# Performance work log

Measured on AMD Instinct MI355X. Metric: run time of the kernel, lower is better.

Reference implementation:

```python
import jax, jax.numpy as jnp
import numpy as np

B, L, E, H, D, DFF = 2, 2048, 1024, 16, 64, 4096
SCALE = D ** 0.5


def rmsnorm(x):
    # NOTE: original uses mean(x*x)**0.5 with no eps and no learned scale
    rms = jnp.sqrt(jnp.mean(x * x, axis=-1, keepdims=True))
    return x / rms


def alibi_matrix():
    i = jnp.arange(L)
    dists = -jnp.abs(i[None, :] - i[:, None]).astype(jnp.float32)  # [L, L]
    slopes = 2.0 ** (-jnp.linspace(1.0, 8.0, H))                   # [H]
    alibi = slopes[:, None, None] * dists                          # [H, L, L]
    causal = jnp.tril(jnp.ones((L, L), dtype=bool))
    return jnp.where(causal[None], alibi, -jnp.inf)[None]          # [1, H, L, L]


def setup_inputs() -> dict:
    key = jax.random.key(0)
    ks = jax.random.split(key, 16)
    s = 0.02
    return {
        "X": jax.random.normal(ks[0], (B, L, E), jnp.float32),
        "encoder_out": jax.random.normal(ks[1], (B, L, E), jnp.float32),
        # self-attention params
        "Wqkv": jax.random.normal(ks[2], (E, 3 * H * D), jnp.float32) * s,
        "bqkv": jnp.zeros((3 * H * D,), jnp.float32),
        "Wo_sa": jax.random.normal(ks[3], (H * D, E), jnp.float32) * s,
        "bo_sa": jnp.zeros((E,), jnp.float32),
        # cross-attention params (computed by torch module but its forward returns X, so unused)
        "Wq": jax.random.normal(ks[4], (E, H * D), jnp.float32) * s,
        "bq": jnp.zeros((H * D,), jnp.float32),
        "Wkv": jax.random.normal(ks[5], (E, 2 * H * D), jnp.float32) * s,
        "bkv": jnp.zeros((2 * H * D,), jnp.float32),
        "Wo_ca": jax.random.normal(ks[6], (H * D, E), jnp.float32) * s,
        "bo_ca": jnp.zeros((E,), jnp.float32),
        # GLU FFN params (bias=False)
        "Ww": jax.random.normal(ks[7], (E, DFF), jnp.float32) * s,
        "Wv": jax.random.normal(ks[8], (E, DFF), jnp.float32) * s,
        "Wout": jax.random.normal(ks[9], (DFF, E), jnp.float32) * s,
    }


def reference(X, encoder_out, Wqkv, bqkv, Wo_sa, bo_sa, Wq, bq, Wkv, bkv,
              Wo_ca, bo_ca, Ww, Wv, Wout):
    alibi = alibi_matrix()

    # ---- self-attention (pre-norm + residual) ----
    h = rmsnorm(X)
    qkv = (h @ Wqkv + bqkv).reshape(B, L, H, 3, D)
    Q, K, V = qkv[..., 0, :], qkv[..., 1, :], qkv[..., 2, :]      # [B, L, H, D]
    scores = jnp.einsum('blhd,bmhd->bhlm', Q, K) / SCALE + alibi  # [B, H, L, L]
    attn = jax.nn.softmax(scores, axis=-1)
    ctx = jnp.einsum('bhlm,bmhd->blhd', attn, V).reshape(B, L, H * D)
    X = X + ctx @ Wo_sa + bo_sa

    # ---- cross-attention stage ----
    # Faithful to source: CrossAttention.forward returns its input X (the
    # normalized tensor) rather than the attention output, so this block is
    # X + rmsnorm(X). Cross-attn params never affect the output.
    X = X + rmsnorm(X)

    # ---- GLU FFN (pre-norm + residual), exact (erf) GELU as in torch F.gelu ----
    h = rmsnorm(X)
    ff = jax.nn.gelu(h @ Ww, approximate=False) * (h @ Wv)
    X = X + ff @ Wout
    return X
```

## Files before the change

kernel.cpp:

```cpp
#include <hip/hip_runtime.h>

#define B_SZ 2
#define L_SEQ 2048
#define E_DIM 1024
#define NH 16
#define DH 64
#define DFF_DIM 4096
#define ROWS (B_SZ * L_SEQ)
#define NCID 80

typedef __attribute__((ext_vector_type(8))) short short8;
typedef __attribute__((ext_vector_type(4))) float f32x4;

__device__ __forceinline__ short f2bf(float f) {
  unsigned u = __builtin_bit_cast(unsigned, f);
  u = (u + 0x7FFFu + ((u >> 16) & 1u)) >> 16;
  return (short)u;
}
__device__ __forceinline__ float bf2f(short s) {
  unsigned u = ((unsigned)(unsigned short)s) << 16;
  return __builtin_bit_cast(float, u);
}

__device__ __forceinline__ float fast_gelu(float x) {
  float ax = fabsf(x) * 0.70710678118654752f;
  float t = __builtin_amdgcn_rcpf(__builtin_fmaf(0.3275911f, ax, 1.0f));
  float p = t * __builtin_fmaf(
                    t,
                    __builtin_fmaf(
                        t,
                        __builtin_fmaf(t,
                                       __builtin_fmaf(t, 1.061405429f,
                                                      -1.453152027f),
                                       1.421413741f),
                        -0.284496736f),
                    0.254829592f);
  float erf = 1.0f - p * __expf(-ax * ax);
  erf = copysignf(erf, x);
  return 0.5f * x * (1.0f + erf);
}

__device__ __forceinline__ void async_copy16(const void* g, void* l) {
  __builtin_amdgcn_global_load_lds(
      (const __attribute__((address_space(1))) void*)g,
      (__attribute__((address_space(3))) void*)l, 16, 0, 0);
}

__device__ __forceinline__ float block_sum256(float v) {
  __shared__ float sbuf[4];
#pragma unroll
  for (int off = 32; off > 0; off >>= 1) v += __shfl_xor(v, off, 64);
  int lane = threadIdx.x & 63, w = threadIdx.x >> 6;
  if (lane == 0) sbuf[w] = v;
  __syncthreads();
  return sbuf[0] + sbuf[1] + sbuf[2] + sbuf[3];
}

__global__ __launch_bounds__(256) void prep_all(
    const float* __restrict__ Wqkv, const float* __restrict__ Wo,
    const float* __restrict__ Ww, const float* __restrict__ Wv,
    const float* __restrict__ Wout, const float* __restrict__ X,
    short* __restrict__ Bqkv3, short* __restrict__ WoT,
    short* __restrict__ Bcat, short* __restrict__ WoutT,
    short* __restrict__ H) {
  __shared__ float tile[32][33];
  int b = blockIdx.x;
  if (b < 16384) {
    const float* W;
    short* Wt;
    int K, N, mode, bx, by;
    if (b < 3072) {
      W = Wqkv; Wt = Bqkv3; K = 1024; N = 3072; mode = 1;
      bx = b % 96; by = b / 96;
    } else if (b < 4096) {
      int c = b - 3072;
      W = Wo; Wt = WoT; K = 1024; N = 1024; mode = 1;
      bx = c & 31; by = c >> 5;
    } else if (b < 8192) {
      int c = b - 4096;
      W = Ww; Wt = Bcat; K = 1024; N = 4096; mode = 2;
      bx = c & 127; by = c >> 7;
    } else if (b < 12288) {
      int c = b - 8192;
      W = Wv; Wt = Bcat; K = 1024; N = 4096; mode = 3;
      bx = c & 127; by = c >> 7;
    } else {
      int c = b - 12288;
      W = Wout; Wt = WoutT; K = 4096; N = 1024; mode = 1;
      bx = c & 31; by = c >> 5;
    }
    int n0 = bx * 32, k0 = by * 32;
    int tx = threadIdx.x & 31, ty = threadIdx.x >> 5;
#pragma unroll
    for (int i = 0; i < 4; i++)
      tile[ty + 8 * i][tx] = W[(size_t)(k0 + ty + 8 * i) * N + n0 + tx];
    __syncthreads();
#pragma unroll
    for (int i = 0; i < 4; i++) {
      int n = n0 + ty + 8 * i;
      int orow = (mode == 1)
                     ? n
                     : ((n >> 5) * 64 + (n & 31) + (mode == 3 ? 32 : 0));
      Wt[(size_t)orow * K + k0 + tx] = f2bf(tile[tx][ty + 8 * i]);
    }
  } else {
    size_t row = b - 16384;
    float4 v = ((const float4*)(X + row * E_DIM))[threadIdx.x];
    float ss = v.x * v.x + v.y * v.y + v.z * v.z + v.w * v.w;
    ss = block_sum256(ss);
    float inv = rsqrtf(ss * (1.0f / E_DIM));
    short* h = H + row * E_DIM + (size_t)threadIdx.x * 4;
    h[0] = f2bf(v.x * inv);
    h[1] = f2bf(v.y * inv);
    h[2] = f2bf(v.z * inv);
    h[3] = f2bf(v.w * inv);
  }
}

__global__ __launch_bounds__(256) void resid_rms_fused(
    const float* __restrict__ X, const float* __restrict__ P0,
    const float* __restrict__ P1, const float* __restrict__ bias,
    float* __restrict__ Xout, short* __restrict__ H) {
  size_t row = blockIdx.x;
  int t = threadIdx.x;
  float4 v = ((const float4*)(X + row * E_DIM))[t];
  float4 a = ((const float4*)(P0 + row * E_DIM))[t];
  float4 b = ((const float4*)(P1 + row * E_DIM))[t];
  float4 c = ((const float4*)bias)[t];
  v.x += a.x + b.x + c.x;
  v.y += a.y + b.y + c.y;
  v.z += a.z + b.z + c.z;
  v.w += a.w + b.w + c.w;
  float ss = v.x * v.x + v.y * v.y + v.z * v.z + v.w * v.w;
  ss = block_sum256(ss);
  float inv = rsqrtf(ss * (1.0f / E_DIM));
  float4 o;
  o.x = v.x * (1.0f + inv);
  o.y = v.y * (1.0f + inv);
  o.z = v.z * (1.0f + inv);
  o.w = v.w * (1.0f + inv);
  ((float4*)(Xout + row * E_DIM))[t] = o;
  short* h = H + row * E_DIM + (size_t)t * 4;
  h[0] = f2bf(v.x * inv);
  h[1] = f2bf(v.y * inv);
  h[2] = f2bf(v.z * inv);
  h[3] = f2bf(v.w * inv);
}

__global__ __launch_bounds__(256) void add2_k(const float* __restrict__ P0,
                                              const float* __restrict__ P1,
                                              float* __restrict__ out) {
  size_t i = (size_t)blockIdx.x * 256 + threadIdx.x;
  float4 v = ((const float4*)out)[i];
  float4 a = ((const float4*)P0)[i];
  float4 b = ((const float4*)P1)[i];
  v.x += a.x + b.x;
  v.y += a.y + b.y;
  v.z += a.z + b.z;
  v.w += a.w + b.w;
  ((float4*)out)[i] = v;
}

__global__ __launch_bounds__(256, 2) void gemm_bt(
    const short* __restrict__ A, const short* __restrict__ Bt,
    const float* __restrict__ bias, void* __restrict__ out,
    void* __restrict__ out2, void* __restrict__ out3, int M, int N, int K,
    int epi, int ksplit) {
  __shared__ short smem[128 * 32 * 4];
  short* As0 = smem;
  short* Bs0 = smem + 4096;
  short* As1 = smem + 8192;
  short* Bs1 = smem + 12288;
  int t = threadIdx.x;
  int lane = t & 63;
  int quad = lane >> 4, l16 = lane & 15;
  int wave = t >> 6;
  int wr = wave >> 1, wc = wave & 1;
  int m0 = blockIdx.y * 128, n0 = blockIdx.x * 128;
  int klen = K / ksplit;
  int kstart = blockIdx.z * klen;

  f32x4 acc[4][4];
#pragma unroll
  for (int i = 0; i < 4; i++)
#pragma unroll
    for (int j = 0; j < 4; j++) acc[i][j] = (f32x4){0.f, 0.f, 0.f, 0.f};

  for (int k0 = kstart; k0 < kstart + klen; k0 += 64) {
    __syncthreads();
#pragma unroll
    for (int p = 0; p < 2; p++) {
      int s = p * 256 + t;
      int mm = s >> 2, kk = (s & 3) * 8;
      const short* ag = A + (size_t)(m0 + mm) * K + k0 + kk;
      const short* bg = Bt + (size_t)(n0 + mm) * K + k0 + kk;
      async_copy16(ag, As0 + (size_t)s * 8);
      async_copy16(bg, Bs0 + (size_t)s * 8);
      async_copy16(ag + 32, As1 + (size_t)s * 8);
      async_copy16(bg + 32, Bs1 + (size_t)s * 8);
    }
    __syncthreads();
#pragma unroll
    for (int half = 0; half < 2; half++) {
      const short* As = half ? As1 : As0;
      const short* Bs = half ? Bs1 : Bs0;
      short8 af[4], bfv[4];
#pragma unroll
      for (int i = 0; i < 4; i++) {
        af[i] = *(const short8*)&As[(wr * 64 + i * 16 + l16) * 32 + quad * 8];
        bfv[i] = *(const short8*)&Bs[(wc * 64 + i * 16 + l16) * 32 + quad * 8];
      }
#pragma unroll
      for (int mi = 0; mi < 4; mi++)
#pragma unroll
        for (int ni = 0; ni < 4; ni++)
          acc[mi][ni] = __builtin_amdgcn_mfma_f32_16x16x32_bf16(
              af[mi], bfv[ni], acc[mi][ni], 0, 0, 0);
    }
  }

  if (epi == 5) {
    short* FF = (short*)out;
    int ffbase = blockIdx.x * 64 + wc * 32;
#pragma unroll
    for (int mi = 0; mi < 4; mi++)
#pragma unroll
      for (int ni = 0; ni < 2; ni++)
#pragma unroll
        for (int r = 0; r < 4; r++) {
          int rowl = wr * 64 + mi * 16 + quad * 4 + r;
          float g = fast_gelu(acc[mi][ni][r]);
          FF[(size_t)(m0 + rowl) * DFF_DIM + ffbase + ni * 16 + l16] =
              f2bf(g * acc[mi][ni + 2][r]);
        }
    return;
  }

#pragma unroll
  for (int mi = 0; mi < 4; mi++) {
#pragma unroll
    for (int ni = 0; ni < 4; ni++) {
      int col = n0 + wc * 64 + ni * 16 + l16;
#pragma unroll
      for (int r = 0; r < 4; r++) {
        int row = m0 + wr * 64 + mi * 16 + quad * 4 + r;
        float v = acc[mi][ni][r];
        if (epi == 4) {
          float* po = (float*)out + (size_t)blockIdx.z * ((size_t)M * N);
          po[(size_t)row * N + col] = v;
        } else {
          v += bias[col];
          int h = col / 192;
          int rem = col - h * 192;
          int ty = rem >> 6, d = rem & 63;
          short* dst = (ty == 0) ? (short*)out
                                 : ((ty == 1) ? (short*)out2 : (short*)out3);
          int bb = row >> 11, l = row & 2047;
          dst[((size_t)(bb * NH + h) * L_SEQ + l) * DH + d] = f2bf(v);
        }
      }
    }
  }
}

__global__ __launch_bounds__(256) void v_transp(const short* __restrict__ Vh,
                                                short* __restrict__ VTh) {
  int lt = blockIdx.x, bh = blockIdx.y;
  __shared__ short vtile[64 * 72];
  int t = threadIdx.x;
  int r = t >> 3, c = (t & 7) * 8;
  const short* src = Vh + ((size_t)bh * L_SEQ + lt * 64) * DH;
#pragma unroll
  for (int p = 0; p < 2; p++) {
    int row = r + p * 32;
    short8 vv = *(const short8*)(src + (size_t)row * DH + c);
    *(short8*)&vtile[row * 72 + c] = vv;
  }
  __syncthreads();
#pragma unroll
  for (int p = 0; p < 2; p++) {
    int d = r + p * 32;
    short8 o;
#pragma unroll
    for (int u = 0; u < 8; u++) o[u] = vtile[(c + u) * 72 + d];
    *(short8*)(VTh + ((size_t)bh * DH + d) * L_SEQ + lt * 64 + c) = o;
  }
}

__global__ __launch_bounds__(256) void attn_k(const short* __restrict__ Qh,
                                              const short* __restrict__ Kh,
                                              const short* __restrict__ VTh,
                                              float* __restrict__ OP,
                                              float* __restrict__ RS) {
  int cid = blockIdx.x;
  int bh = blockIdx.y;
  int b = bh >> 4, h = bh & 15;
  int qt, ch;
  if (cid < 8) {
    qt = cid; ch = 0;
  } else if (cid < 24) {
    qt = 8 + ((cid - 8) >> 1); ch = (cid - 8) & 1;
  } else if (cid < 48) {
    qt = 16 + (cid - 24) / 3; ch = (cid - 24) % 3;
  } else {
    qt = 24 + ((cid - 48) >> 2); ch = (cid - 48) & 3;
  }
  int t0 = ch * 8;
  int tend = min(t0 + 8, qt + 1);

  int t = threadIdx.x;
  int wave = t >> 6, lane = t & 63;
  int quad = lane >> 4, l16 = lane & 15;

  __shared__ short kt[64 * 72];
  __shared__ short vt[64 * 72];
  __shared__ short pb[4 * 16 * 70];

  const float slope = exp2f(-(1.0f + (7.0f / 15.0f) * (float)h));
  int iw = qt * 64 + wave * 16;

  short8 qf[2];
  {
    const short* qp = Qh + ((size_t)bh * L_SEQ + iw + l16) * DH + quad * 8;
    qf[0] = *(const short8*)(qp);
    qf[1] = *(const short8*)(qp + 32);
  }

  f32x4 o[4];
#pragma unroll
  for (int i = 0; i < 4; i++) o[i] = (f32x4){0.f, 0.f, 0.f, 0.f};
  float rs[4] = {0.f, 0.f, 0.f, 0.f};
  float crow[4];
  int irow[4];
#pragma unroll
  for (int r = 0; r < 4; r++) {
    irow[r] = iw + quad * 4 + r;
    crow[r] = -slope * (float)irow[r] - 8.0f;
  }

  int sr = t >> 3, sc = (t & 7) * 8;
  const short* kg = Kh + (size_t)bh * L_SEQ * DH;
  const short* vg = VTh + (size_t)bh * DH * L_SEQ;
  short8 kreg[2], vreg[2];
  auto loadKV = [&](int j0) {
    kreg[0] = *(const short8*)(kg + (size_t)(j0 + sr) * DH + sc);
    kreg[1] = *(const short8*)(kg + (size_t)(j0 + sr + 32) * DH + sc);
    vreg[0] = *(const short8*)(vg + (size_t)sr * L_SEQ + j0 + sc);
    vreg[1] = *(const short8*)(vg + (size_t)(sr + 32) * L_SEQ + j0 + sc);
  };
  loadKV(t0 * 64);

  short* pw = &pb[wave * 16 * 70];
  for (int tix = t0; tix < tend; ++tix) {
    int j0 = tix * 64;
    __syncthreads();
    *(short8*)&kt[sr * 72 + sc] = kreg[0];
    *(short8*)&kt[(sr + 32) * 72 + sc] = kreg[1];
    *(short8*)&vt[sr * 72 + sc] = vreg[0];
    *(short8*)&vt[(sr + 32) * 72 + sc] = vreg[1];
    __syncthreads();
    if (tix + 1 < tend) loadKV(j0 + 64);

    f32x4 s[4];
#pragma unroll
    for (int nt = 0; nt < 4; nt++) {
      f32x4 a = (f32x4){0.f, 0.f, 0.f, 0.f};
#pragma unroll
      for (int ks = 0; ks < 2; ks++) {
        short8 bf =
            *(const short8*)&kt[(nt * 16 + l16) * 72 + ks * 32 + quad * 8];
        a = __builtin_amdgcn_mfma_f32_16x16x32_bf16(qf[ks], bf, a, 0, 0, 0);
      }
      s[nt] = a;
    }
    bool diag = (tix == qt);
#pragma unroll
    for (int nt = 0; nt < 4; nt++) {
      int j = j0 + nt * 16 + l16;
      float jb = slope * (float)j;
#pragma unroll
      for (int r = 0; r < 4; r++) {
        float v = __builtin_fmaf(s[nt][r], 0.125f, jb + crow[r]);
        if (diag && j > irow[r]) v = -1e30f;
        float p = __expf(v);
        rs[r] += p;
        pw[(quad * 4 + r) * 70 + nt * 16 + l16] = f2bf(p);
      }
    }
    short8 pf[2];
    pf[0] = *(const short8*)&pw[l16 * 70 + quad * 8];
    pf[1] = *(const short8*)&pw[l16 * 70 + 32 + quad * 8];
#pragma unroll
    for (int nt = 0; nt < 4; nt++) {
#pragma unroll
      for (int ks = 0; ks < 2; ks++) {
        short8 bv =
            *(const short8*)&vt[(nt * 16 + l16) * 72 + ks * 32 + quad * 8];
        o[nt] = __builtin_amdgcn_mfma_f32_16x16x32_bf16(pf[ks], bv, o[nt], 0,
                                                        0, 0);
      }
    }
  }
  float* op = OP + ((size_t)bh * NCID + cid) * 64 * 64;
  float* rsp = RS + ((size_t)bh * NCID + cid) * 64;
#pragma unroll
  for (int r = 0; r < 4; r++) {
#pragma unroll
    for (int off = 1; off < 16; off <<= 1) rs[r] += __shfl_xor(rs[r], off, 64);
    int rowl = wave * 16 + quad * 4 + r;
#pragma unroll
    for (int nt = 0; nt < 4; nt++) op[rowl * 64 + nt * 16 + l16] = o[nt][r];
    if (l16 == 0) rsp[rowl] = rs[r];
  }
}

__global__ __launch_bounds__(256) void attn_merge(const float* __restrict__ OP,
                                                  const float* __restrict__ RS,
                                                  short* __restrict__ ctx) {
  int row = blockIdx.x;
  int b = row >> 11, i = row & 2047;
  int qt = i >> 6, rowin = i & 63;
  int base, nch;
  if (qt < 8) {
    base = qt; nch = 1;
  } else if (qt < 16) {
    base = 8 + 2 * (qt - 8); nch = 2;
  } else if (qt < 24) {
    base = 24 + 3 * (qt - 16); nch = 3;
  } else {
    base = 48 + 4 * (qt - 24); nch = 4;
  }
  int t = threadIdx.x;
  int col = t * 4;
  int h = col >> 6;
  int bh = b * NH + h;
  float4 o = {0.f, 0.f, 0.f, 0.f};
  float l = 0.f;
  for (int s = 0; s < nch; s++) {
    size_t cb = ((size_t)bh * NCID + base + s) * 64 + rowin;
    float4 v = *(const float4*)&OP[cb * 64 + (col & 63)];
    o.x += v.x;
    o.y += v.y;
    o.z += v.z;
    o.w += v.w;
    l += RS[cb];
  }
  float inv = 1.0f / l;
  short* dst = ctx + (size_t)row * (NH * DH) + col;
  dst[0] = f2bf(o.x * inv);
  dst[1] = f2bf(o.y * inv);
  dst[2] = f2bf(o.z * inv);
  dst[3] = f2bf(o.w * inv);
}

extern "C" void kernel_launch(void* const* d_in, const int* in_sizes, int n_in,
                              void* d_out, int out_size, void* d_ws,
                              size_t ws_size, hipStream_t stream) {
  const float* X = (const float*)d_in[0];
  const float* Wqkv = (const float*)d_in[2];
  const float* bqkv = (const float*)d_in[3];
  const float* Wo_sa = (const float*)d_in[4];
  const float* bo_sa = (const float*)d_in[5];
  const float* Ww = (const float*)d_in[12];
  const float* Wv = (const float*)d_in[13];
  const float* Wout = (const float*)d_in[14];

  char* ws = (char*)d_ws;
  auto take = [&](size_t bytes) {
    char* p = ws;
    ws += (bytes + 255) & ~(size_t)255;
    return p;
  };
  short* Bqkv3 = (short*)take((size_t)3072 * 1024 * 2);
  short* WoT = (short*)take((size_t)E_DIM * E_DIM * 2);
  short* Bcat = (short*)take((size_t)2 * DFF_DIM * E_DIM * 2);
  short* WoutT = (short*)take((size_t)E_DIM * DFF_DIM * 2);
  short* Hbuf = (short*)take((size_t)ROWS * E_DIM * 2);
  short* Qh = (short*)take((size_t)ROWS * NH * DH * 2);
  short* Kh = (short*)take((size_t)ROWS * NH * DH * 2);
  short* Vh = (short*)take((size_t)ROWS * NH * DH * 2);
  short* VTh = (short*)take((size_t)ROWS * NH * DH * 2);
  short* CTX = (short*)take((size_t)ROWS * NH * DH * 2);
  char* big = take((size_t)48 * 1024 * 1024);
  float* OP = (float*)big;
  float* RS = OP + (size_t)B_SZ * NH * NCID * 64 * 64;
  float* Pwo = (float*)(big + (size_t)16 * 1024 * 1024);
  short* FF = (short*)Pwo;
  float* Pwout = (float*)Qh;
  (void)ws_size;
  (void)in_sizes;
  (void)n_in;
  (void)out_size;

  dim3 blk(256);
  prep_all<<<16384 + ROWS, blk, 0, stream>>>(Wqkv, Wo_sa, Ww, Wv, Wout, X,
                                             Bqkv3, WoT, Bcat, WoutT, Hbuf);
  gemm_bt<<<dim3(3072 / 128, ROWS / 128), blk, 0, stream>>>(
      Hbuf, Bqkv3, bqkv, Qh, Kh, Vh, ROWS, 3072, 1024, 6, 1);
  v_transp<<<dim3(L_SEQ / 64, B_SZ * NH), blk, 0, stream>>>(Vh, VTh);
  attn_k<<<dim3(NCID, B_SZ * NH), blk, 0, stream>>>(Qh, Kh, VTh, OP, RS);
  attn_merge<<<ROWS, blk, 0, stream>>>(OP, RS, CTX);
  gemm_bt<<<dim3(1024 / 128, ROWS / 128, 2), blk, 0, stream>>>(
      CTX, WoT, nullptr, Pwo, nullptr, nullptr, ROWS, 1024, 1024, 4, 2);
  resid_rms_fused<<<ROWS, blk, 0, stream>>>(
      X, Pwo, Pwo + (size_t)ROWS * E_DIM, bo_sa, (float*)d_out, Hbuf);
  gemm_bt<<<dim3(2 * DFF_DIM / 128, ROWS / 128), blk, 0, stream>>>(
      Hbuf, Bcat, nullptr, FF, nullptr, nullptr, ROWS, 2 * DFF_DIM, 1024, 5,
      1);
  gemm_bt<<<dim3(1024 / 128, ROWS / 128, 2), blk, 0, stream>>>(
      FF, WoutT, nullptr, Pwout, nullptr, nullptr, ROWS, 1024, 4096, 4, 2);
  add2_k<<<ROWS * E_DIM / (256 * 4), blk, 0, stream>>>(
      Pwout, Pwout + (size_t)ROWS * E_DIM, (float*)d_out);
}
```

Before: 421.6 us.

## Add 256x256-tile pipelined MFMA GEMM for QKV and GLU up-projections

Introduces a new 512-thread GEMM kernel with 256x256 output tiles and 128-deep K steps. It uses swizzled LDS staging with async global-to-LDS copies, an 8-phase software pipeline interleaving loads with bf16 MFMAs, and s_setprio around the compute. It replaces the 128-tile gemm_bt for the QKV projection (head-split bias epilogue) and the fused GELU-gated FFN up-projection, to raise arithmetic intensity per byte of LDS and global traffic. The kernel uses 128KB of LDS, so one block fits per CU. The QKV launch also gets fewer blocks than there are CUs, which risks lower occupancy and poor load balance.

```diff
diff --git a/kernel.cpp b/kernel.cpp
--- a/kernel.cpp
+++ b/kernel.cpp
@@ -263,6 +263,163 @@
   }
 }
 
+__global__ __launch_bounds__(512, 2) void gemm256(
+    const short* __restrict__ A, const short* __restrict__ Bt,
+    const float* __restrict__ bias, void* __restrict__ out,
+    void* __restrict__ out2, void* __restrict__ out3, int M, int N, int K,
+    int epi) {
+  __shared__ __align__(16) short smem[65536];
+  (void)M;
+  (void)N;
+  int t = threadIdx.x;
+  int lane = t & 63;
+  int quad = lane >> 4, l16 = lane & 15;
+  int wave = t >> 6;
+  int wr = wave >> 2;
+  int wc = wave & 3;
+  int m0 = blockIdx.y * 256, n0 = blockIdx.x * 256;
+
+  int row0 = t >> 3;
+  int sl = (t & 7) ^ (row0 & 7);
+  int goff = row0 * K + sl * 8;
+  int ldw = t * 16;
+  char* smc = (char*)smem;
+  auto stageHT = [&](const short* gsrc, int ldsbase) {
+    async_copy16(gsrc + goff, smc + ldsbase + ldw);
+    async_copy16(gsrc + goff + (K << 6), smc + ldsbase + 8192 + ldw);
+  };
+
+  int swz = (l16 & 7) << 4;
+  int colp0 = (quad * 16) ^ swz;
+  int colp1 = (64 + quad * 16) ^ swz;
+  const char* aB = smc + wr * 16384 + l16 * 128;
+  const char* bB = smc + 32768 + (wc >> 1) * 16384 + (wc & 1) * 8192 +
+                   l16 * 128;
+
+  f32x4 acc[8][4];
+#pragma unroll
+  for (int i = 0; i < 8; i++)
+#pragma unroll
+    for (int j = 0; j < 4; j++) acc[i][j] = (f32x4){0.f, 0.f, 0.f, 0.f};
+  short8 areg[4][2], breg[4][2];
+
+  const short* Am0 = A + (size_t)m0 * K;
+  const short* Am1 = A + (size_t)(m0 + 128) * K;
+  const short* Bn0 = Bt + (size_t)n0 * K;
+  const short* Bn1 = Bt + (size_t)(n0 + 128) * K;
+
+  stageHT(Am0, 0);
+  stageHT(Am1, 16384);
+  stageHT(Bn0, 32768);
+  stageHT(Bn1, 49152);
+  stageHT(Bn0 + 64, 98304);
+  stageHT(Bn1 + 64, 114688);
+  asm volatile("s_waitcnt vmcnt(4)" ::: "memory");
+  __builtin_amdgcn_s_barrier();
+
+  int NJ = K >> 7;
+  for (int j = 0; j < NJ; ++j) {
+    int kb = j << 7;
+    bool lastI = (j == NJ - 1);
+#pragma unroll
+    for (int ph = 0; ph < 8; ++ph) {
+      const int sub = ph & 3;
+      const int mq = sub >> 1;
+      const int nq = sub & 1;
+      const int dOff = (ph >> 2) ? 65536 : 0;
+      if (sub == 0 || sub == 2) {
+#pragma unroll
+        for (int im = 0; im < 4; ++im) {
+          areg[im][0] =
+              *(const short8*)(aB + dOff + (mq * 4 + im) * 2048 + colp0);
+          areg[im][1] =
+              *(const short8*)(aB + dOff + (mq * 4 + im) * 2048 + colp1);
+        }
+      }
+      if (sub <= 1) {
+#pragma unroll
+        for (int in = 0; in < 2; ++in) {
+          breg[nq * 2 + in][0] =
+              *(const short8*)(bB + dOff + (nq * 2 + in) * 2048 + colp0);
+          breg[nq * 2 + in][1] =
+              *(const short8*)(bB + dOff + (nq * 2 + in) * 2048 + colp1);
+        }
+      }
+      if (ph == 0) stageHT(Am0 + kb + 64, 65536);
+      if (ph == 1) stageHT(Am1 + kb + 64, 65536 + 16384);
+      if (!lastI) {
+        if (ph == 2) stageHT(Bn0 + kb + 128, 32768);
+        if (ph == 3) stageHT(Bn1 + kb + 128, 49152);
+        if (ph == 4) stageHT(Am0 + kb + 128, 0);
+        if (ph == 5) stageHT(Am1 + kb + 128, 16384);
+        if (ph == 6) stageHT(Bn0 + kb + 192, 98304);
+        if (ph == 7) stageHT(Bn1 + kb + 192, 114688);
+      }
+      __builtin_amdgcn_s_barrier();
+      asm volatile("s_waitcnt lgkmcnt(0)" ::: "memory");
+      __builtin_amdgcn_sched_barrier(0);
+      __builtin_amdgcn_s_setprio(1);
+#pragma unroll
+      for (int im = 0; im < 4; ++im)
+#pragma unroll
+        for (int in = 0; in < 2; ++in)
+#pragma unroll
+          for (int kh = 0; kh < 2; ++kh)
+            acc[mq * 4 + im][nq * 2 + in] =
+                __builtin_amdgcn_mfma_f32_16x16x32_bf16(
+                    areg[im][kh], breg[nq * 2 + in][kh],
+                    acc[mq * 4 + im][nq * 2 + in], 0, 0, 0);
+      __builtin_amdgcn_s_setprio(0);
+      if (ph == 3) {
+        if (lastI)
+          asm volatile("s_waitcnt vmcnt(0)" ::: "memory");
+        else
+          asm volatile("s_waitcnt vmcnt(4)" ::: "memory");
+      }
+      if (ph == 7 && !lastI)
+        asm volatile("s_waitcnt vmcnt(4)" ::: "memory");
+      __builtin_amdgcn_s_barrier();
+    }
+  }
+
+  if (epi == 5) {
+    short* FF = (short*)out;
+    int ffbase = (n0 + wc * 64) >> 1;
+#pragma unroll
+    for (int mi = 0; mi < 8; ++mi)
+#pragma unroll
+      for (int ni = 0; ni < 2; ++ni)
+#pragma unroll
+        for (int r = 0; r < 4; ++r) {
+          int rowl = wr * 128 + mi * 16 + quad * 4 + r;
+          float g = fast_gelu(acc[mi][ni][r]);
+          FF[(size_t)(m0 + rowl) * DFF_DIM + ffbase + ni * 16 + l16] =
+              f2bf(g * acc[mi][ni + 2][r]);
+        }
+    return;
+  }
+#pragma unroll
+  for (int mi = 0; mi < 8; ++mi) {
+#pragma unroll
+    for (int ni = 0; ni < 4; ++ni) {
+      int col = n0 + wc * 64 + ni * 16 + l16;
+      float bv = bias[col];
+      int h = col / 192;
+      int rem = col - h * 192;
+      int ty = rem >> 6, d = rem & 63;
+      short* dst =
+          (ty == 0) ? (short*)out : ((ty == 1) ? (short*)out2 : (short*)out3);
+#pragma unroll
+      for (int r = 0; r < 4; ++r) {
+        int row = m0 + wr * 128 + mi * 16 + quad * 4 + r;
+        float v = acc[mi][ni][r] + bv;
+        int bb = row >> 11, l = row & 2047;
+        dst[((size_t)(bb * NH + h) * L_SEQ + l) * DH + d] = f2bf(v);
+      }
+    }
+  }
+}
+
 __global__ __launch_bounds__(256) void v_transp(const short* __restrict__ Vh,
                                                 short* __restrict__ VTh) {
   int lt = blockIdx.x, bh = blockIdx.y;
@@ -495,8 +652,8 @@
   dim3 blk(256);
   prep_all<<<16384 + ROWS, blk, 0, stream>>>(Wqkv, Wo_sa, Ww, Wv, Wout, X,
                                              Bqkv3, WoT, Bcat, WoutT, Hbuf);
-  gemm_bt<<<dim3(3072 / 128, ROWS / 128), blk, 0, stream>>>(
-      Hbuf, Bqkv3, bqkv, Qh, Kh, Vh, ROWS, 3072, 1024, 6, 1);
+  gemm256<<<dim3(3072 / 256, ROWS / 256), dim3(512), 0, stream>>>(
+      Hbuf, Bqkv3, bqkv, Qh, Kh, Vh, ROWS, 3072, 1024, 6);
   v_transp<<<dim3(L_SEQ / 64, B_SZ * NH), blk, 0, stream>>>(Vh, VTh);
   attn_k<<<dim3(NCID, B_SZ * NH), blk, 0, stream>>>(Qh, Kh, VTh, OP, RS);
   attn_merge<<<ROWS, blk, 0, stream>>>(OP, RS, CTX);
@@ -504,9 +661,8 @@
       CTX, WoT, nullptr, Pwo, nullptr, nullptr, ROWS, 1024, 1024, 4, 2);
   resid_rms_fused<<<ROWS, blk, 0, stream>>>(
       X, Pwo, Pwo + (size_t)ROWS * E_DIM, bo_sa, (float*)d_out, Hbuf);
-  gemm_bt<<<dim3(2 * DFF_DIM / 128, ROWS / 128), blk, 0, stream>>>(
-      Hbuf, Bcat, nullptr, FF, nullptr, nullptr, ROWS, 2 * DFF_DIM, 1024, 5,
-      1);
+  gemm256<<<dim3(2 * DFF_DIM / 256, ROWS / 256), dim3(512), 0, stream>>>(
+      Hbuf, Bcat, nullptr, FF, nullptr, nullptr, ROWS, 2 * DFF_DIM, 1024, 5);
   gemm_bt<<<dim3(1024 / 128, ROWS / 128, 2), blk, 0, stream>>>(
       FF, WoutT, nullptr, Pwout, nullptr, nullptr, ROWS, 1024, 4096, 4, 2);
   add2_k<<<ROWS * E_DIM / (256 * 4), blk, 0, stream>>>(
```

After: 413.0 us. 2.0% less time.
